# Optimization experiments

Hardware: AMD Instinct MI355X
Metric: run time of the kernel (lower is better)

The kernel has to match this reference:

```python
import math
import jax, jax.numpy as jnp
import numpy as np

DIM = 384
NUM_HEADS = 12
KS = 7
GROUP_WIDTH = 8
LAM = 1.0
GAMMA = 1.0
DIM_QK = DIM // 3 * 2  # 256, multiple of group_width
DIM_V = DIM
SCALE = (DIM // NUM_HEADS) ** -0.5
GROUPS = DIM_QK // GROUP_WIDTH  # 32


def setup_inputs() -> dict:
    key = jax.random.key(0)
    ks = jax.random.split(key, 10)
    B_, N = 32, 196
    x = jax.random.normal(ks[0], (B_, N, DIM), dtype=jnp.float32)
    qkv_out = DIM_QK * 2 + DIM_V  # 704
    w_qkv = jax.random.normal(ks[1], (qkv_out, DIM), dtype=jnp.float32) * 0.02
    b_qkv = jnp.zeros((qkv_out,), dtype=jnp.float32)
    # grouped 7x7 conv: (out=DIM_QK, in_per_group=GROUP_WIDTH, KS, KS)
    w_dw = jax.random.normal(ks[2], (DIM_QK, GROUP_WIDTH, KS, KS), dtype=jnp.float32) * 0.05
    b_dw = jnp.zeros((DIM_QK,), dtype=jnp.float32)
    # 1x1 conv to KS^2 * num_heads channels
    w_pw = jax.random.normal(ks[3], (KS * KS * NUM_HEADS, DIM_QK), dtype=jnp.float32) * 0.05
    b_pw = jnp.zeros((KS * KS * NUM_HEADS,), dtype=jnp.float32)
    # ghost head: cat(ghost_mul ~ randn, ghost_add ~ trunc_normal(0.02)) -> (2,1,DIM_V,KS,KS)
    ghost_mul = jax.random.normal(ks[4], (1, 1, DIM_V, KS, KS), dtype=jnp.float32)
    ghost_add = jax.random.normal(ks[5], (1, 1, DIM_V, KS, KS), dtype=jnp.float32) * 0.02
    ghost_head = jnp.concatenate((ghost_mul, ghost_add), axis=0)
    w_proj = jax.random.normal(ks[6], (DIM, DIM_V), dtype=jnp.float32) * 0.02
    b_proj = jnp.zeros((DIM,), dtype=jnp.float32)
    return {"x": x, "w_qkv": w_qkv, "b_qkv": b_qkv, "w_dw": w_dw, "b_dw": b_dw,
            "w_pw": w_pw, "b_pw": b_pw, "ghost_head": ghost_head,
            "w_proj": w_proj, "b_proj": b_proj}


def reference(x, w_qkv, b_qkv, w_dw, b_dw, w_pw, b_pw, ghost_head, w_proj, b_proj):
    B, N, C = x.shape
    H = W = int(math.sqrt(N))
    G, Cg, ks = NUM_HEADS, DIM_V // NUM_HEADS, KS

    qkv = jnp.einsum('bnc,oc->bno', x, w_qkv) + b_qkv
    q, k, v = jnp.split(qkv, (DIM_QK, 2 * DIM_QK), axis=-1)
    q = jnp.transpose(q, (0, 2, 1)).reshape(B, DIM_QK, H, W)
    k = jnp.transpose(k, (0, 2, 1)).reshape(B, DIM_QK, H, W)
    v = jnp.transpose(v, (0, 2, 1)).reshape(B, DIM_V, H, W)

    # Hadamard QK interaction + attention-map generator
    hp = q * k * SCALE
    pad = ks // 2
    h = jax.lax.conv_general_dilated(
        hp, w_dw, window_strides=(1, 1), padding=((pad, pad), (pad, pad)),
        feature_group_count=GROUPS, dimension_numbers=('NCHW', 'OIHW', 'NCHW'))
    h = h + b_dw[None, :, None, None]
    h = jax.nn.gelu(h, approximate=False)
    h = jnp.einsum('bchw,oc->bohw', h, w_pw) + b_pw[None, :, None, None]  # (B, ks^2*G, H, W)

    h_attn = jax.nn.softmax(h.reshape(B * G, ks * ks, H, W), axis=1)
    v_g = v.reshape(B * G, Cg, H, W)

    # ghost heads (broadcast over batch, split channels into heads)
    gh = jnp.broadcast_to(ghost_head, (2, B, DIM_V, ks, ks)).reshape(2, B * G, Cg, ks * ks)
    ghost_mul = gh[0] ** LAM        # (BG, Cg, ks^2)
    ghost_add = gh[1] * GAMMA       # (BG, Cg, ks^2)

    # elsa_op: windowed weighted sum (unfold equivalent, torch channel-major order)
    vp = jnp.pad(v_g, ((0, 0), (0, 0), (pad, pad), (pad, pad)))
    patches = jnp.stack([vp[:, :, i:i + H, j:j + W]
                         for i in range(ks) for j in range(ks)], axis=2)  # (BG, Cg, ks^2, H, W)
    filt = (ghost_mul[:, :, :, None, None] * h_attn[:, None, :, :, :]
            + ghost_add[:, :, :, None, None])
    out = (patches * filt).sum(axis=2)  # (BG, Cg, H, W)

    out = out.reshape(B, DIM_V, H, W).transpose(0, 2, 3, 1).reshape(B, N, DIM_V)
    y = jnp.einsum('bnc,oc->bno', out, w_proj) + b_proj
    return y
```

## Files before the change

### kernel.cpp

```cpp
#include <hip/hip_runtime.h>
#include <hip/hip_bf16.h>

#define B_    32
#define N_    196
#define H_    14
#define DIMC  384
#define DQK   256
#define DV    384
#define NH    12
#define CG    32
#define NPW   588
#define PAD_  3
#define SCALE_ 0.17677669529663687f

typedef __bf16 bf16x8 __attribute__((ext_vector_type(8)));
typedef float  f32x4  __attribute__((ext_vector_type(4)));

__device__ inline bf16x8 bf16x8_zero() {
    bf16x8 z;
    #pragma unroll
    for (int j = 0; j < 8; ++j) z[j] = (__bf16)0.0f;
    return z;
}

__device__ inline void split2(float v, __hip_bfloat16& h, __hip_bfloat16& l) {
    h = __float2bfloat16(v);
    l = __float2bfloat16(v - __bfloat162float(h));
}

__global__ __launch_bounds__(256) void k_split(
    const float* __restrict__ s0, const float* __restrict__ s1,
    const float* __restrict__ s2, const float* __restrict__ s3,
    __hip_bfloat16* __restrict__ h0, __hip_bfloat16* __restrict__ l0,
    __hip_bfloat16* __restrict__ h1, __hip_bfloat16* __restrict__ l1,
    __hip_bfloat16* __restrict__ h2, __hip_bfloat16* __restrict__ l2,
    __hip_bfloat16* __restrict__ h3, __hip_bfloat16* __restrict__ l3)
{
    int i = blockIdx.x * 256 + threadIdx.x;
    if (i >= 762624) return;
    const float* src; __hip_bfloat16 *dh, *dl; int off;
    if      (i < 602112) { src = s0; dh = h0; dl = l0; off = i; }
    else if (i < 688128) { src = s1; dh = h1; dl = l1; off = i - 602112; }
    else if (i < 725760) { src = s2; dh = h2; dl = l2; off = i - 688128; }
    else                 { src = s3; dh = h3; dl = l3; off = i - 725760; }
    const float4 v = ((const float4*)src)[off];
    union { __hip_bfloat16 b[4]; uint2 u; } H, L;
    split2(v.x, H.b[0], L.b[0]); split2(v.y, H.b[1], L.b[1]);
    split2(v.z, H.b[2], L.b[2]); split2(v.w, H.b[3], L.b[3]);
    ((uint2*)dh)[off] = H.u;
    ((uint2*)dl)[off] = L.u;
}

template<int EPI>
__global__ __launch_bounds__(256) void k_mfma(
    const __hip_bfloat16* __restrict__ Phi, const __hip_bfloat16* __restrict__ Plo,
    const __hip_bfloat16* __restrict__ Qhi, const __hip_bfloat16* __restrict__ Qlo,
    const float* __restrict__ bias, int K, int nQ,
    float* __restrict__ out0, float* __restrict__ out1, float* __restrict__ out2)
{
    __shared__ ushort lds[16384];
    const int t    = threadIdx.x;
    const int m0   = blockIdx.x * 128;
    const int n0   = blockIdx.y * 128;
    const int lane = t & 63;
    const int wv   = t >> 6;
    const int wm   = (wv >> 1) * 64;
    const int wn   = (wv & 1) * 64;
    const int l16  = lane & 15;
    const int kb   = lane >> 4;

    f32x4 acc[4][4];
    #pragma unroll
    for (int mi = 0; mi < 4; ++mi)
        #pragma unroll
        for (int nj = 0; nj < 4; ++nj) acc[mi][nj] = f32x4{0.f, 0.f, 0.f, 0.f};

    for (int k0 = 0; k0 < K; k0 += 32) {
        bf16x8 rA[2][2], rB[2][2];
        #pragma unroll
        for (int q = 0; q < 2; ++q) {
            const int u = q * 256 + t;
            const int r = u >> 2;
            const int kk = (u & 3) * 8;
            const size_t pOff = (size_t)(m0 + r) * K + k0 + kk;
            rA[q][0] = *(const bf16x8*)(Phi + pOff);
            rA[q][1] = *(const bf16x8*)(Plo + pOff);
            if (n0 + r < nQ) {
                const size_t qOff = (size_t)(n0 + r) * K + k0 + kk;
                rB[q][0] = *(const bf16x8*)(Qhi + qOff);
                rB[q][1] = *(const bf16x8*)(Qlo + qOff);
            } else { rB[q][0] = bf16x8_zero(); rB[q][1] = bf16x8_zero(); }
        }
        __syncthreads();
        #pragma unroll
        for (int q = 0; q < 2; ++q) {
            const int u  = q * 256 + t;
            const int r  = u >> 2;
            const int sw = ((u << 4) ^ ((r & 7) << 4)) >> 1;
            *(bf16x8*)&lds[sw]         = rA[q][0];
            *(bf16x8*)&lds[sw + 4096]  = rA[q][1];
            *(bf16x8*)&lds[sw + 8192]  = rB[q][0];
            *(bf16x8*)&lds[sw + 12288] = rB[q][1];
        }
        __syncthreads();
        bf16x8 bh[4], bl[4];
        #pragma unroll
        for (int nj = 0; nj < 4; ++nj) {
            const int br  = wn + nj * 16 + l16;
            const int idx = ((br * 64 + kb * 16) ^ ((br & 7) << 4)) >> 1;
            bh[nj] = *(const bf16x8*)&lds[8192 + idx];
            bl[nj] = *(const bf16x8*)&lds[12288 + idx];
        }
        #pragma unroll
        for (int mi = 0; mi < 4; ++mi) {
            const int ar  = wm + mi * 16 + l16;
            const int idx = ((ar * 64 + kb * 16) ^ ((ar & 7) << 4)) >> 1;
            const bf16x8 ah = *(const bf16x8*)&lds[idx];
            const bf16x8 al = *(const bf16x8*)&lds[4096 + idx];
            #pragma unroll
            for (int nj = 0; nj < 4; ++nj) {
                acc[mi][nj] = __builtin_amdgcn_mfma_f32_16x16x32_bf16(ah, bh[nj], acc[mi][nj], 0, 0, 0);
                acc[mi][nj] = __builtin_amdgcn_mfma_f32_16x16x32_bf16(ah, bl[nj], acc[mi][nj], 0, 0, 0);
                acc[mi][nj] = __builtin_amdgcn_mfma_f32_16x16x32_bf16(al, bh[nj], acc[mi][nj], 0, 0, 0);
            }
        }
    }

    #pragma unroll
    for (int mi = 0; mi < 4; ++mi) {
        #pragma unroll
        for (int r = 0; r < 4; ++r) {
            const int m = m0 + wm + mi * 16 + kb * 4 + r;
            #pragma unroll
            for (int nj = 0; nj < 4; ++nj) {
                const int col = n0 + wn + nj * 16 + l16;
                const float v = acc[mi][nj][r];
                if (EPI == 0) {
                    const float val = v + bias[col];
                    const int bb = m / N_, n = m - bb * N_;
                    if (col < DQK)          out0[((size_t)bb * DQK + col) * N_ + n] = val;
                    else if (col < 2*DQK)   out1[((size_t)bb * DQK + (col - DQK)) * N_ + n] = val;
                    else                    out2[((size_t)bb * DV + (col - 2*DQK)) * N_ + n] = val;
                } else if (EPI == 1) {
                    if (col < NPW) out0[(size_t)m * NPW + col] = v + bias[col];
                } else {
                    out0[(size_t)m * DV + col] = v + bias[col];
                }
            }
        }
    }
}

__global__ __launch_bounds__(256) void k_dwconv(const float* __restrict__ qT,
    const float* __restrict__ kT, const float* __restrict__ w_dw,
    const float* __restrict__ b_dw,
    __hip_bfloat16* __restrict__ h1t_hi, __hip_bfloat16* __restrict__ h1t_lo)
{
    const int b  = blockIdx.x;
    const int gp = blockIdx.y;
    __shared__ float hp[16 * 400];
    __shared__ float wsm[16 * 392];
    const int t = threadIdx.x;
    for (int i = t; i < 16 * 400; i += 256) hp[i] = 0.f;
    for (int i = t; i < 16 * 392; i += 256) wsm[i] = w_dw[gp * 6272 + i];
    __syncthreads();
    for (int i = t; i < 16 * N_; i += 256) {
        const int cl = i / N_;
        const int n  = i - cl * N_;
        const int y  = n / H_, x = n - y * H_;
        const size_t gi = ((size_t)b * DQK + gp * 16 + cl) * N_ + n;
        hp[cl * 400 + (y + PAD_) * 20 + (x + PAD_)] = qT[gi] * kT[gi] * SCALE_;
    }
    __syncthreads();
    if (t < 224) {
        const int od = t / 14;
        const int y  = t - od * 14;
        const int icb = (od >> 3) << 3;
        float acc[14];
        #pragma unroll
        for (int x = 0; x < 14; ++x) acc[x] = 0.f;
        for (int ic = 0; ic < 8; ++ic) {
            const float* hrow = &hp[(icb + ic) * 400];
            const float* wrow = &wsm[od * 392 + ic * 49];
            #pragma unroll
            for (int ky = 0; ky < 7; ++ky) {
                float r[20];
                #pragma unroll
                for (int ii = 0; ii < 20; ii += 4)
                    *(float4*)&r[ii] = *(const float4*)&hrow[(y + ky) * 20 + ii];
                #pragma unroll
                for (int kx = 0; kx < 7; ++kx) {
                    const float wv = wrow[ky * 7 + kx];
                    #pragma unroll
                    for (int x = 0; x < 14; ++x)
                        acc[x] += r[x + kx] * wv;
                }
            }
        }
        const float bv = b_dw[gp * 16 + od];
        const int c = gp * 16 + od;
        #pragma unroll
        for (int x = 0; x < 14; ++x) {
            const float s  = acc[x] + bv;
            const float gv = 0.5f * s * (1.f + erff(s * 0.70710678118654752440f));
            __hip_bfloat16 hb, lb; split2(gv, hb, lb);
            const size_t o = ((size_t)b * N_ + y * H_ + x) * DQK + c;
            h1t_hi[o] = hb; h1t_lo[o] = lb;
        }
    }
}

__global__ __launch_bounds__(256) void k_elsa(const float* __restrict__ h2t,
    const float* __restrict__ vT, const float* __restrict__ ghost,
    __hip_bfloat16* __restrict__ orm_hi, __hip_bfloat16* __restrict__ orm_lo)
{
    const int b  = blockIdx.x;
    const int g  = blockIdx.y;
    const int c0 = blockIdx.z * 8;
    __shared__ float vp[8 * 400];
    __shared__ float gmga[8 * 49 * 2];
    const int t = threadIdx.x;

    for (int i = t; i < 8 * 400; i += 256) vp[i] = 0.f;
    for (int i = t; i < 8 * 49; i += 256) {
        const int c = i / 49, p = i - c * 49;
        gmga[(c * 49 + p) * 2 + 0] = ghost[(size_t)(g * CG + c0 + c) * 49 + p];
        gmga[(c * 49 + p) * 2 + 1] = ghost[(size_t)DV * 49 + (g * CG + c0 + c) * 49 + p];
    }
    __syncthreads();
    for (int i = t; i < 8 * N_; i += 256) {
        const int c = i / N_;
        const int n = i - c * N_;
        const int y = n / H_, x = n - y * H_;
        vp[c * 400 + (y + PAD_) * 20 + (x + PAD_)] =
            vT[((size_t)b * DV + g * CG + c0 + c) * N_ + n];
    }
    __syncthreads();

    if (t < N_) {
        const int n = t;
        const int y = n / H_, x = n - y * H_;
        const int base = y * 20 + x;
        const size_t m = (size_t)b * N_ + n;

        const float* hr = h2t + m * NPW + g * 49;
        float a[49];
        #pragma unroll
        for (int p = 0; p < 49; ++p) a[p] = hr[p];
        float mx = -1e30f;
        #pragma unroll
        for (int p = 0; p < 49; ++p) mx = fmaxf(mx, a[p]);
        float ssum = 0.f;
        #pragma unroll
        for (int p = 0; p < 49; ++p) { a[p] = expf(a[p] - mx); ssum += a[p]; }
        const float inv = 1.f / ssum;
        #pragma unroll
        for (int p = 0; p < 49; ++p) a[p] *= inv;

        #pragma unroll 1
        for (int c = 0; c < 8; ++c) {
            const float* vrow = &vp[c * 400 + base];
            const float* gg   = &gmga[c * 98];
            float s = 0.f;
            #pragma unroll
            for (int ky = 0; ky < 7; ++ky)
                #pragma unroll
                for (int kx = 0; kx < 7; ++kx) {
                    const int p = ky * 7 + kx;
                    s += vrow[ky * 20 + kx] * (gg[p * 2] * a[p] + gg[p * 2 + 1]);
                }
            __hip_bfloat16 hb, lb; split2(s, hb, lb);
            const size_t o = m * DV + g * CG + c0 + c;
            orm_hi[o] = hb; orm_lo[o] = lb;
        }
    }
}

extern "C" void kernel_launch(void* const* d_in, const int* in_sizes, int n_in,
                              void* d_out, int out_size, void* d_ws, size_t ws_size,
                              hipStream_t stream)
{
    const float* x      = (const float*)d_in[0];
    const float* w_qkv  = (const float*)d_in[1];
    const float* b_qkv  = (const float*)d_in[2];
    const float* w_dw   = (const float*)d_in[3];
    const float* b_dw   = (const float*)d_in[4];
    const float* w_pw   = (const float*)d_in[5];
    const float* b_pw   = (const float*)d_in[6];
    const float* ghost  = (const float*)d_in[7];
    const float* w_proj = (const float*)d_in[8];
    const float* b_proj = (const float*)d_in[9];
    float* y  = (float*)d_out;
    char* ws = (char*)d_ws;

    __hip_bfloat16* x_hi     = (__hip_bfloat16*)(ws + 0);
    __hip_bfloat16* x_lo     = (__hip_bfloat16*)(ws + 4816896);
    __hip_bfloat16* wqkv_hi  = (__hip_bfloat16*)(ws + 9633792);
    __hip_bfloat16* wqkv_lo  = (__hip_bfloat16*)(ws + 10321920);
    float*          h2t      = (float*)         (ws + 0);
    float*          qT       = (float*)         (ws + 14751744);
    float*          kT       = (float*)         (ws + 21174272);
    __hip_bfloat16* orm_hi   = (__hip_bfloat16*)(ws + 14751744);
    __hip_bfloat16* orm_lo   = (__hip_bfloat16*)(ws + 19568640);
    float*          vT       = (float*)         (ws + 27596800);
    __hip_bfloat16* wpw_hi   = (__hip_bfloat16*)(ws + 37230592);
    __hip_bfloat16* wpw_lo   = (__hip_bfloat16*)(ws + 37531648);
    __hip_bfloat16* wproj_hi = (__hip_bfloat16*)(ws + 37832704);
    __hip_bfloat16* wproj_lo = (__hip_bfloat16*)(ws + 38127616);
    __hip_bfloat16* h1t_hi   = (__hip_bfloat16*)(ws + 38422528);
    __hip_bfloat16* h1t_lo   = (__hip_bfloat16*)(ws + 41633792);

    k_split<<<2979, 256, 0, stream>>>(x, w_qkv, w_pw, w_proj,
        x_hi, x_lo, wqkv_hi, wqkv_lo, wpw_hi, wpw_lo, wproj_hi, wproj_lo);

    k_mfma<0><<<dim3(49, 7), 256, 0, stream>>>(x_hi, x_lo, wqkv_hi, wqkv_lo,
        b_qkv, DIMC, 896, qT, kT, vT);

    k_dwconv<<<dim3(32, 16), 256, 0, stream>>>(qT, kT, w_dw, b_dw, h1t_hi, h1t_lo);

    k_mfma<1><<<dim3(49, 5), 256, 0, stream>>>(h1t_hi, h1t_lo, wpw_hi, wpw_lo,
        b_pw, DQK, NPW, h2t, nullptr, nullptr);

    k_elsa<<<dim3(32, 12, 4), 256, 0, stream>>>(h2t, vT, ghost, orm_hi, orm_lo);

    k_mfma<2><<<dim3(49, 3), 256, 0, stream>>>(orm_hi, orm_lo, wproj_hi, wproj_lo,
        b_proj, DV, DV, y, nullptr, nullptr);
}
```

Before: 241.9 us.

## Drop split-bf16 three-pass GEMMs for single bf16 MFMA and transpose attention logits

Replaces the hi/lo bf16 split emulation of fp32 GEMMs with plain single bf16 operands. Each k-step now issues one MFMA instead of three, and global loads, LDS traffic and intermediate writes are halved. The pointwise-conv GEMM output is also written channel-major, so the ELSA kernel's per-pixel softmax reads are coalesced across threads. The cost is lower accuracy: all three projections now run at plain bf16 precision, which may exceed the tolerance.

```diff
diff --git a/kernel.cpp b/kernel.cpp
--- a/kernel.cpp
+++ b/kernel.cpp
@@ -23,42 +23,33 @@
     return z;
 }
 
-__device__ inline void split2(float v, __hip_bfloat16& h, __hip_bfloat16& l) {
-    h = __float2bfloat16(v);
-    l = __float2bfloat16(v - __bfloat162float(h));
-}
-
 __global__ __launch_bounds__(256) void k_split(
     const float* __restrict__ s0, const float* __restrict__ s1,
     const float* __restrict__ s2, const float* __restrict__ s3,
-    __hip_bfloat16* __restrict__ h0, __hip_bfloat16* __restrict__ l0,
-    __hip_bfloat16* __restrict__ h1, __hip_bfloat16* __restrict__ l1,
-    __hip_bfloat16* __restrict__ h2, __hip_bfloat16* __restrict__ l2,
-    __hip_bfloat16* __restrict__ h3, __hip_bfloat16* __restrict__ l3)
+    __hip_bfloat16* __restrict__ d0, __hip_bfloat16* __restrict__ d1,
+    __hip_bfloat16* __restrict__ d2, __hip_bfloat16* __restrict__ d3)
 {
     int i = blockIdx.x * 256 + threadIdx.x;
     if (i >= 762624) return;
-    const float* src; __hip_bfloat16 *dh, *dl; int off;
-    if      (i < 602112) { src = s0; dh = h0; dl = l0; off = i; }
-    else if (i < 688128) { src = s1; dh = h1; dl = l1; off = i - 602112; }
-    else if (i < 725760) { src = s2; dh = h2; dl = l2; off = i - 688128; }
-    else                 { src = s3; dh = h3; dl = l3; off = i - 725760; }
+    const float* src; __hip_bfloat16* dst; int off;
+    if      (i < 602112) { src = s0; dst = d0; off = i; }
+    else if (i < 688128) { src = s1; dst = d1; off = i - 602112; }
+    else if (i < 725760) { src = s2; dst = d2; off = i - 688128; }
+    else                 { src = s3; dst = d3; off = i - 725760; }
     const float4 v = ((const float4*)src)[off];
-    union { __hip_bfloat16 b[4]; uint2 u; } H, L;
-    split2(v.x, H.b[0], L.b[0]); split2(v.y, H.b[1], L.b[1]);
-    split2(v.z, H.b[2], L.b[2]); split2(v.w, H.b[3], L.b[3]);
-    ((uint2*)dh)[off] = H.u;
-    ((uint2*)dl)[off] = L.u;
+    union { __hip_bfloat16 b[4]; uint2 u; } Hh;
+    Hh.b[0] = __float2bfloat16(v.x); Hh.b[1] = __float2bfloat16(v.y);
+    Hh.b[2] = __float2bfloat16(v.z); Hh.b[3] = __float2bfloat16(v.w);
+    ((uint2*)dst)[off] = Hh.u;
 }
 
 template<int EPI>
 __global__ __launch_bounds__(256) void k_mfma(
-    const __hip_bfloat16* __restrict__ Phi, const __hip_bfloat16* __restrict__ Plo,
-    const __hip_bfloat16* __restrict__ Qhi, const __hip_bfloat16* __restrict__ Qlo,
+    const __hip_bfloat16* __restrict__ P, const __hip_bfloat16* __restrict__ Q,
     const float* __restrict__ bias, int K, int nQ,
     float* __restrict__ out0, float* __restrict__ out1, float* __restrict__ out2)
 {
-    __shared__ ushort lds[16384];
+    __shared__ ushort lds[8192];
     const int t    = threadIdx.x;
     const int m0   = blockIdx.x * 128;
     const int n0   = blockIdx.y * 128;
@@ -76,20 +67,16 @@
         for (int nj = 0; nj < 4; ++nj) acc[mi][nj] = f32x4{0.f, 0.f, 0.f, 0.f};
 
     for (int k0 = 0; k0 < K; k0 += 32) {
-        bf16x8 rA[2][2], rB[2][2];
+        bf16x8 rA[2], rB[2];
         #pragma unroll
         for (int q = 0; q < 2; ++q) {
             const int u = q * 256 + t;
             const int r = u >> 2;
             const int kk = (u & 3) * 8;
-            const size_t pOff = (size_t)(m0 + r) * K + k0 + kk;
-            rA[q][0] = *(const bf16x8*)(Phi + pOff);
-            rA[q][1] = *(const bf16x8*)(Plo + pOff);
-            if (n0 + r < nQ) {
-                const size_t qOff = (size_t)(n0 + r) * K + k0 + kk;
-                rB[q][0] = *(const bf16x8*)(Qhi + qOff);
-                rB[q][1] = *(const bf16x8*)(Qlo + qOff);
-            } else { rB[q][0] = bf16x8_zero(); rB[q][1] = bf16x8_zero(); }
+            rA[q] = *(const bf16x8*)(P + (size_t)(m0 + r) * K + k0 + kk);
+            rB[q] = (n0 + r < nQ)
+                  ? *(const bf16x8*)(Q + (size_t)(n0 + r) * K + k0 + kk)
+                  : bf16x8_zero();
         }
         __syncthreads();
         #pragma unroll
@@ -97,32 +84,25 @@
             const int u  = q * 256 + t;
             const int r  = u >> 2;
             const int sw = ((u << 4) ^ ((r & 7) << 4)) >> 1;
-            *(bf16x8*)&lds[sw]         = rA[q][0];
-            *(bf16x8*)&lds[sw + 4096]  = rA[q][1];
-            *(bf16x8*)&lds[sw + 8192]  = rB[q][0];
-            *(bf16x8*)&lds[sw + 12288] = rB[q][1];
+            *(bf16x8*)&lds[sw]        = rA[q];
+            *(bf16x8*)&lds[sw + 4096] = rB[q];
         }
         __syncthreads();
-        bf16x8 bh[4], bl[4];
+        bf16x8 bh[4];
         #pragma unroll
         for (int nj = 0; nj < 4; ++nj) {
             const int br  = wn + nj * 16 + l16;
             const int idx = ((br * 64 + kb * 16) ^ ((br & 7) << 4)) >> 1;
-            bh[nj] = *(const bf16x8*)&lds[8192 + idx];
-            bl[nj] = *(const bf16x8*)&lds[12288 + idx];
+            bh[nj] = *(const bf16x8*)&lds[4096 + idx];
         }
         #pragma unroll
         for (int mi = 0; mi < 4; ++mi) {
             const int ar  = wm + mi * 16 + l16;
             const int idx = ((ar * 64 + kb * 16) ^ ((ar & 7) << 4)) >> 1;
             const bf16x8 ah = *(const bf16x8*)&lds[idx];
-            const bf16x8 al = *(const bf16x8*)&lds[4096 + idx];
             #pragma unroll
-            for (int nj = 0; nj < 4; ++nj) {
+            for (int nj = 0; nj < 4; ++nj)
                 acc[mi][nj] = __builtin_amdgcn_mfma_f32_16x16x32_bf16(ah, bh[nj], acc[mi][nj], 0, 0, 0);
-                acc[mi][nj] = __builtin_amdgcn_mfma_f32_16x16x32_bf16(ah, bl[nj], acc[mi][nj], 0, 0, 0);
-                acc[mi][nj] = __builtin_amdgcn_mfma_f32_16x16x32_bf16(al, bh[nj], acc[mi][nj], 0, 0, 0);
-            }
         }
     }
 
@@ -142,7 +122,10 @@
                     else if (col < 2*DQK)   out1[((size_t)bb * DQK + (col - DQK)) * N_ + n] = val;
                     else                    out2[((size_t)bb * DV + (col - 2*DQK)) * N_ + n] = val;
                 } else if (EPI == 1) {
-                    if (col < NPW) out0[(size_t)m * NPW + col] = v + bias[col];
+                    if (col < NPW) {
+                        const int bb = m / N_, n = m - bb * N_;
+                        out0[((size_t)bb * NPW + col) * N_ + n] = v + bias[col];
+                    }
                 } else {
                     out0[(size_t)m * DV + col] = v + bias[col];
                 }
@@ -153,8 +136,7 @@
 
 __global__ __launch_bounds__(256) void k_dwconv(const float* __restrict__ qT,
     const float* __restrict__ kT, const float* __restrict__ w_dw,
-    const float* __restrict__ b_dw,
-    __hip_bfloat16* __restrict__ h1t_hi, __hip_bfloat16* __restrict__ h1t_lo)
+    const float* __restrict__ b_dw, __hip_bfloat16* __restrict__ h1t)
 {
     const int b  = blockIdx.x;
     const int gp = blockIdx.y;
@@ -203,16 +185,14 @@
         for (int x = 0; x < 14; ++x) {
             const float s  = acc[x] + bv;
             const float gv = 0.5f * s * (1.f + erff(s * 0.70710678118654752440f));
-            __hip_bfloat16 hb, lb; split2(gv, hb, lb);
-            const size_t o = ((size_t)b * N_ + y * H_ + x) * DQK + c;
-            h1t_hi[o] = hb; h1t_lo[o] = lb;
-        }
-    }
-}
-
-__global__ __launch_bounds__(256) void k_elsa(const float* __restrict__ h2t,
+            h1t[((size_t)b * N_ + y * H_ + x) * DQK + c] = __float2bfloat16(gv);
+        }
+    }
+}
+
+__global__ __launch_bounds__(256) void k_elsa(const float* __restrict__ h2c,
     const float* __restrict__ vT, const float* __restrict__ ghost,
-    __hip_bfloat16* __restrict__ orm_hi, __hip_bfloat16* __restrict__ orm_lo)
+    __hip_bfloat16* __restrict__ orm)
 {
     const int b  = blockIdx.x;
     const int g  = blockIdx.y;
@@ -241,12 +221,11 @@
         const int n = t;
         const int y = n / H_, x = n - y * H_;
         const int base = y * 20 + x;
-        const size_t m = (size_t)b * N_ + n;
-
-        const float* hr = h2t + m * NPW + g * 49;
+
+        const float* hr = h2c + ((size_t)b * NPW + g * 49) * N_ + n;
         float a[49];
         #pragma unroll
-        for (int p = 0; p < 49; ++p) a[p] = hr[p];
+        for (int p = 0; p < 49; ++p) a[p] = hr[(size_t)p * N_];
         float mx = -1e30f;
         #pragma unroll
         for (int p = 0; p < 49; ++p) mx = fmaxf(mx, a[p]);
@@ -257,6 +236,7 @@
         #pragma unroll
         for (int p = 0; p < 49; ++p) a[p] *= inv;
 
+        const size_t m = (size_t)b * N_ + n;
         #pragma unroll 1
         for (int c = 0; c < 8; ++c) {
             const float* vrow = &vp[c * 400 + base];
@@ -269,9 +249,7 @@
                     const int p = ky * 7 + kx;
                     s += vrow[ky * 20 + kx] * (gg[p * 2] * a[p] + gg[p * 2 + 1]);
                 }
-            __hip_bfloat16 hb, lb; split2(s, hb, lb);
-            const size_t o = m * DV + g * CG + c0 + c;
-            orm_hi[o] = hb; orm_lo[o] = lb;
+            orm[m * DV + g * CG + c0 + c] = __float2bfloat16(s);
         }
     }
 }
@@ -293,36 +271,30 @@
     float* y  = (float*)d_out;
     char* ws = (char*)d_ws;
 
-    __hip_bfloat16* x_hi     = (__hip_bfloat16*)(ws + 0);
-    __hip_bfloat16* x_lo     = (__hip_bfloat16*)(ws + 4816896);
-    __hip_bfloat16* wqkv_hi  = (__hip_bfloat16*)(ws + 9633792);
-    __hip_bfloat16* wqkv_lo  = (__hip_bfloat16*)(ws + 10321920);
-    float*          h2t      = (float*)         (ws + 0);
+    __hip_bfloat16* x_bf     = (__hip_bfloat16*)(ws + 0);
+    __hip_bfloat16* wqkv_bf  = (__hip_bfloat16*)(ws + 4816896);
+    float*          h2c      = (float*)         (ws + 0);
     float*          qT       = (float*)         (ws + 14751744);
     float*          kT       = (float*)         (ws + 21174272);
-    __hip_bfloat16* orm_hi   = (__hip_bfloat16*)(ws + 14751744);
-    __hip_bfloat16* orm_lo   = (__hip_bfloat16*)(ws + 19568640);
+    __hip_bfloat16* orm_bf   = (__hip_bfloat16*)(ws + 14751744);
     float*          vT       = (float*)         (ws + 27596800);
-    __hip_bfloat16* wpw_hi   = (__hip_bfloat16*)(ws + 37230592);
-    __hip_bfloat16* wpw_lo   = (__hip_bfloat16*)(ws + 37531648);
-    __hip_bfloat16* wproj_hi = (__hip_bfloat16*)(ws + 37832704);
-    __hip_bfloat16* wproj_lo = (__hip_bfloat16*)(ws + 38127616);
-    __hip_bfloat16* h1t_hi   = (__hip_bfloat16*)(ws + 38422528);
-    __hip_bfloat16* h1t_lo   = (__hip_bfloat16*)(ws + 41633792);
+    __hip_bfloat16* wpw_bf   = (__hip_bfloat16*)(ws + 37230592);
+    __hip_bfloat16* wproj_bf = (__hip_bfloat16*)(ws + 37531648);
+    __hip_bfloat16* h1t_bf   = (__hip_bfloat16*)(ws + 37826560);
 
     k_split<<<2979, 256, 0, stream>>>(x, w_qkv, w_pw, w_proj,
-        x_hi, x_lo, wqkv_hi, wqkv_lo, wpw_hi, wpw_lo, wproj_hi, wproj_lo);
-
-    k_mfma<0><<<dim3(49, 7), 256, 0, stream>>>(x_hi, x_lo, wqkv_hi, wqkv_lo,
+        x_bf, wqkv_bf, wpw_bf, wproj_bf);
+
+    k_mfma<0><<<dim3(49, 7), 256, 0, stream>>>(x_bf, wqkv_bf,
         b_qkv, DIMC, 896, qT, kT, vT);
 
-    k_dwconv<<<dim3(32, 16), 256, 0, stream>>>(qT, kT, w_dw, b_dw, h1t_hi, h1t_lo);
-
-    k_mfma<1><<<dim3(49, 5), 256, 0, stream>>>(h1t_hi, h1t_lo, wpw_hi, wpw_lo,
-        b_pw, DQK, NPW, h2t, nullptr, nullptr);
-
-    k_elsa<<<dim3(32, 12, 4), 256, 0, stream>>>(h2t, vT, ghost, orm_hi, orm_lo);
-
-    k_mfma<2><<<dim3(49, 3), 256, 0, stream>>>(orm_hi, orm_lo, wproj_hi, wproj_lo,
+    k_dwconv<<<dim3(32, 16), 256, 0, stream>>>(qT, kT, w_dw, b_dw, h1t_bf);
+
+    k_mfma<1><<<dim3(49, 5), 256, 0, stream>>>(h1t_bf, wpw_bf,
+        b_pw, DQK, NPW, h2c, nullptr, nullptr);
+
+    k_elsa<<<dim3(32, 12, 4), 256, 0, stream>>>(h2c, vT, ghost, orm_bf);
+
+    k_mfma<2><<<dim3(49, 3), 256, 0, stream>>>(orm_bf, wproj_bf,
         b_proj, DV, DV, y, nullptr, nullptr);
 }
```

Result: faster. 216.6 us (-10.5%).
